# Optimization experiments

Hardware: AMD Instinct MI355X
Metric: run time of the kernel (lower is better)

The kernel has to match this reference:

```python
import jax, jax.numpy as jnp
import numpy as np

TAU = 2.0        # args.tau default (spikingjelly LIFNode)
V_TH = 1.0       # v_threshold
V_RESET = 0.0    # v_reset (hard reset)
ALPHA = 2.0      # ATan surrogate alpha

@jax.custom_vjp
def atan_spike(x):
    # Heaviside spike with ATan surrogate gradient (spikingjelly surrogate.ATan)
    return (x >= 0.0).astype(x.dtype)

def _atan_fwd(x):
    return atan_spike(x), x

def _atan_bwd(x, g):
    sg = (ALPHA / 2.0) / (1.0 + (jnp.pi / 2.0 * ALPHA * x) ** 2)
    return (g * sg,)

atan_spike.defvjp(_atan_fwd, _atan_bwd)

def setup_inputs() -> dict:
    key = jax.random.key(0)
    k1, k2, k3 = jax.random.split(key, 3)
    T, B, IN, OUT, NC = 16, 512, 3072, 2048, 10
    x_seq = jax.random.normal(k1, (T, B, IN), dtype=jnp.float32)
    # xavier-uniform-like scale: sqrt(2/(fan_in+fan_out))
    fc_w = jax.random.normal(k2, (OUT, IN), dtype=jnp.float32) * np.sqrt(2.0 / (IN + OUT)).astype(np.float32)
    fc_b = jnp.zeros((OUT,), jnp.float32)
    aux_w = jax.random.normal(k3, (NC, OUT), dtype=jnp.float32) * np.sqrt(2.0 / (OUT + NC)).astype(np.float32)
    aux_b = jnp.zeros((NC,), jnp.float32)
    return {"x_seq": x_seq, "fc_w": fc_w, "fc_b": fc_b, "aux_w": aux_w, "aux_b": aux_b}

def reference(x_seq, fc_w, fc_b, aux_w, aux_b):
    # fc over all timesteps: [T,B,in] @ [out,in]^T -> [T,B,out]
    cur_seq = jnp.einsum('tbi,oi->tbo', x_seq, fc_w) + fc_b

    def step(v, c):
        # LIF charge: v += (x - (v - v_reset)) / tau
        v = v + (c - (v - V_RESET)) / TAU
        s = atan_spike(v - V_TH)
        s_d = jax.lax.stop_gradient(s)  # detach_reset=True
        v = (1.0 - s_d) * v + s_d * V_RESET  # hard reset
        return v, s

    v0 = jnp.full(cur_seq.shape[1:], V_RESET, cur_seq.dtype)  # reset_net -> v = v_reset
    _, spk_seq = jax.lax.scan(step, v0, cur_seq)  # spk_seq: [T,B,out]
    count = spk_seq.sum(axis=0)                    # [B,out]
    logits = count @ aux_w.T + aux_b               # aux_head local logits [B,10]
    return spk_seq, count, logits
```

## Files before the change

### kernel.cpp

```cpp
#include <hip/hip_runtime.h>
#include <hip/hip_bf16.h>
#include <stdint.h>

#define T_   16
#define B_   512
#define IN_  3072
#define OUT_ 2048
#define NC_  10
#define M_   (T_ * B_)

#define BM 128
#define BN 128

#define SPK_SZ ((size_t)T_ * B_ * OUT_)
#define CNT_SZ ((size_t)B_ * OUT_)

#define TOL 1.2e-4
#define MAXFLAG (B_ * OUT_)

#define BK2   32
#define NCH2  (IN_ / BK2)
#define TILE_US 8192
#define APAN (M_ / BM)
#define BPAN (OUT_ / BN)

#define A_PREP_BLOCKS (APAN * NCH2 * 2)
#define B_PREP_BLOCKS (BPAN * NCH2 * 2)

typedef __attribute__((ext_vector_type(8))) short s16x8;
typedef __attribute__((ext_vector_type(4))) float f32x4;

__device__ unsigned int g_ctr;
__device__ unsigned int g_list[MAXFLAG];

__global__ void zero_ctr() { if (threadIdx.x == 0) g_ctr = 0; }

__device__ __forceinline__ unsigned short f2bf(float f) {
    __bf16 h = (__bf16)f;
    return *(unsigned short*)&h;
}
__device__ __forceinline__ float bf2f(unsigned short u) {
    union { unsigned int i; float f; } c; c.i = ((unsigned int)u) << 16; return c.f;
}
__device__ __forceinline__ int swz8(int r, int g) {
    return r * 64 + ((g ^ (r & 7)) << 3);
}

__device__ __forceinline__ void gload_lds16(const void* g, void* l) {
    __builtin_amdgcn_global_load_lds(
        (const __attribute__((address_space(1))) unsigned int*)g,
        (__attribute__((address_space(3))) unsigned int*)l, 16, 0, 0);
}

__global__ __launch_bounds__(256)
void prep2(const float* __restrict__ x, const float* __restrict__ w,
           unsigned short* __restrict__ Adig, unsigned short* __restrict__ Bdig)
{
    if (blockIdx.x == 0 && threadIdx.x == 0) g_ctr = 0;

    const float* src; unsigned short* dst; int id; bool isA;
    if (blockIdx.x < A_PREP_BLOCKS) {
        src = x; dst = Adig; id = blockIdx.x * 256 + threadIdx.x; isA = true;
    } else {
        src = w; dst = Bdig; id = (blockIdx.x - A_PREP_BLOCKS) * 256 + threadIdx.x; isA = false;
    }
    const int gk = id & 3;
    const int r  = (id >> 2) & 127;
    const int ch = (id >> 9) % NCH2;
    const int pa = id / (NCH2 * 512);
    const int m  = pa * 128 + r;
    const int k  = ch * BK2 + gk * 8;

    size_t srow;
    if (isA) srow = (size_t)(m & 15) * B_ + (m >> 4);
    else     srow = (size_t)m;

    float f[8];
    *(float4*)&f[0] = *(const float4*)(src + srow * IN_ + k);
    *(float4*)&f[4] = *(const float4*)(src + srow * IN_ + k + 4);
    s16x8 hi, lo;
#pragma unroll
    for (int j = 0; j < 8; ++j) {
        unsigned short hb = f2bf(f[j]);
        hi[j] = (short)hb;
        lo[j] = (short)f2bf(f[j] - bf2f(hb));
    }
    unsigned short* tb = dst + ((size_t)pa * NCH2 + ch) * TILE_US;
    *(s16x8*)&tb[swz8(r, gk)]     = hi;
    *(s16x8*)&tb[swz8(r, gk + 4)] = lo;
}

__global__ __launch_bounds__(256, 2)
void gemm_fused(const unsigned short* __restrict__ Adig,
                const unsigned short* __restrict__ Bdig,
                const float* __restrict__ fcb,
                float* __restrict__ out)
{
    __shared__ __align__(16) unsigned short SH[4 * TILE_US];
    unsigned short* Ash0 = SH;
    unsigned short* Bsh0 = SH + 2 * TILE_US;

    const int tid = threadIdx.x;
    const int l   = tid & 63;
    const int wv  = tid >> 6;
    const int wm  = (wv >> 1) * 64;
    const int wn  = (wv & 1) * 64;

    const int lin = blockIdx.x;
    const int xcd = lin & 7;
    const int jj  = lin >> 3;
    const int pm  = xcd * 8 + (jj & 7);
    const int pn  = jj >> 3;
    const int n0  = pn * BN;

    f32x4 acc[4][4];
#pragma unroll
    for (int i = 0; i < 4; ++i)
#pragma unroll
        for (int j = 0; j < 4; ++j) acc[i][j] = (f32x4)0.0f;

    const int lp = l & 15;
    const int lq = l >> 4;
    const int l8 = l * 8;

    const unsigned short* Abase = Adig + (size_t)pm * NCH2 * TILE_US;
    const unsigned short* Bbase = Bdig + (size_t)pn * NCH2 * TILE_US;

    auto stage = [&](int ch, int d) {
        if (wv < 2) {
            const unsigned short* sA = Abase + (size_t)ch * TILE_US + wv * 4096;
            unsigned short* dA = Ash0 + d * TILE_US + wv * 4096;
#pragma unroll
            for (int i = 0; i < 8; ++i)
                gload_lds16(sA + i * 512 + l8, dA + i * 512);
        } else {
            const unsigned short* sB = Bbase + (size_t)ch * TILE_US + (wv - 2) * 4096;
            unsigned short* dB = Bsh0 + d * TILE_US + (wv - 2) * 4096;
#pragma unroll
            for (int i = 0; i < 8; ++i)
                gload_lds16(sB + i * 512 + l8, dB + i * 512);
        }
    };

    stage(0, 0);

    for (int ch = 0; ch < NCH2; ++ch) {
        const int d = ch & 1;
        if (ch + 1 < NCH2) {
            stage(ch + 1, d ^ 1);
            asm volatile("s_waitcnt vmcnt(8)" ::: "memory");
        } else {
            asm volatile("s_waitcnt vmcnt(0)" ::: "memory");
        }
        __builtin_amdgcn_s_barrier();
        asm volatile("" ::: "memory");

        s16x8 a1f[4], a2f[4], b1f[4], b2f[4];
#pragma unroll
        for (int i = 0; i < 4; ++i) {
            const int ra = wm + i * 16 + lp;
            a1f[i] = *(const s16x8*)&Ash0[d * TILE_US + swz8(ra, lq)];
            a2f[i] = *(const s16x8*)&Ash0[d * TILE_US + swz8(ra, lq + 4)];
            const int rb = wn + i * 16 + lp;
            b1f[i] = *(const s16x8*)&Bsh0[d * TILE_US + swz8(rb, lq)];
            b2f[i] = *(const s16x8*)&Bsh0[d * TILE_US + swz8(rb, lq + 4)];
        }

        __builtin_amdgcn_s_setprio(1);
#pragma unroll
        for (int i = 0; i < 4; ++i)
#pragma unroll
            for (int j = 0; j < 4; ++j) {
                acc[i][j] = __builtin_amdgcn_mfma_f32_16x16x32_bf16(
                    a1f[i], b1f[j], acc[i][j], 0, 0, 0);
                acc[i][j] = __builtin_amdgcn_mfma_f32_16x16x32_bf16(
                    a2f[i], b1f[j], acc[i][j], 0, 0, 0);
                acc[i][j] = __builtin_amdgcn_mfma_f32_16x16x32_bf16(
                    a1f[i], b2f[j], acc[i][j], 0, 0, 0);
            }
        __builtin_amdgcn_s_setprio(0);

        asm volatile("s_waitcnt lgkmcnt(0)" ::: "memory");
        __builtin_amdgcn_s_barrier();
        asm volatile("" ::: "memory");
    }

    float* cf = (float*)SH;

    const int crow0 = lq * 4;
#pragma unroll
    for (int i = 0; i < 4; ++i)
#pragma unroll
        for (int j = 0; j < 4; ++j)
#pragma unroll
            for (int reg = 0; reg < 4; ++reg) {
                const int row = wm + i * 16 + crow0 + reg;
                const int col = wn + j * 16 + lp;
                cf[row * 128 + (col ^ ((row & 7) << 2))] = acc[i][j][reg];
            }
    __syncthreads();

    const int o_l = tid & 127;
    const int o   = n0 + o_l;
    const double bias = (double)fcb[o];
    const int bq0 = (tid >> 7) * 4;

#pragma unroll
    for (int q = 0; q < 4; ++q) {
        const int bl = bq0 + q;
        const int b  = pm * 8 + bl;
        double v = 0.0; int cnt = 0; bool fl = false;
#pragma unroll
        for (int t = 0; t < T_; ++t) {
            const int row = bl * 16 + t;
            const float c32 = cf[row * 128 + (o_l ^ ((row & 7) << 2))];
            const double c = (double)c32 + bias;
            v = v + (c - v) * 0.5;
            const double dlt = v - 1.0;
            const bool s = dlt >= 0.0;
            if (fabs(dlt) < TOL) fl = true;
            out[(size_t)t * CNT_SZ + (size_t)b * OUT_ + o] = s ? 1.0f : 0.0f;
            cnt += s ? 1 : 0;
            if (s) v = 0.0;
        }
        out[SPK_SZ + (size_t)b * OUT_ + o] = (float)cnt;
        if (fl) {
            unsigned int idx = atomicAdd(&g_ctr, 1u);
            if (idx < MAXFLAG) g_list[idx] = (unsigned int)(b * OUT_ + o);
        }
    }
}

__global__ __launch_bounds__(256, 2)
void gemm_split(const float* __restrict__ x, const float* __restrict__ w,
                float* __restrict__ cur)
{
    __shared__ __align__(16) unsigned short A1[BM * 64];
    __shared__ __align__(16) unsigned short A2[BM * 64];
    __shared__ __align__(16) unsigned short B1[BN * 64];
    __shared__ __align__(16) unsigned short B2[BN * 64];

    const int tid = threadIdx.x;
    const int l   = tid & 63;
    const int wv  = tid >> 6;
    const int wm  = (wv >> 1) * 64;
    const int wn  = (wv & 1) * 64;
    const int m0  = blockIdx.x * BM;
    const int n0  = blockIdx.y * BN;

    const int r = tid >> 1;
    const int h = tid & 1;
    const float* xa = x + (size_t)(m0 + r) * IN_ + h * 32;
    const float* wa = w + (size_t)(n0 + r) * IN_ + h * 32;

    f32x4 acc[4][4];
#pragma unroll
    for (int i = 0; i < 4; ++i)
#pragma unroll
        for (int j = 0; j < 4; ++j) acc[i][j] = (f32x4)0.0f;

    const int lp = l & 15;
    const int lq = l >> 4;

    for (int ch = 0; ch < 48; ++ch) {
        const int k0 = ch * 64;
        __syncthreads();
        float fx[32], fw[32];
#pragma unroll
        for (int i = 0; i < 8; ++i)
            *(float4*)&fx[4 * i] = *(const float4*)(xa + k0 + 4 * i);
#pragma unroll
        for (int i = 0; i < 8; ++i)
            *(float4*)&fw[4 * i] = *(const float4*)(wa + k0 + 4 * i);

#pragma unroll
        for (int q = 0; q < 4; ++q) {
            s16x8 vh, vl, uh, ul;
#pragma unroll
            for (int j = 0; j < 8; ++j) {
                float f = fx[8 * q + j];
                unsigned short hb = f2bf(f);
                vh[j] = (short)hb;
                vl[j] = (short)f2bf(f - bf2f(hb));
                float g = fw[8 * q + j];
                unsigned short gb = f2bf(g);
                uh[j] = (short)gb;
                ul[j] = (short)f2bf(g - bf2f(gb));
            }
            const int gg = h * 4 + q;
            *(s16x8*)&A1[swz8(r, gg)] = vh;
            *(s16x8*)&A2[swz8(r, gg)] = vl;
            *(s16x8*)&B1[swz8(r, gg)] = uh;
            *(s16x8*)&B2[swz8(r, gg)] = ul;
        }
        __syncthreads();

#pragma unroll
        for (int kk = 0; kk < 2; ++kk) {
            const int gb = kk * 4 + lq;
            s16x8 a1f[4], a2f[4], b1f[4], b2f[4];
#pragma unroll
            for (int i = 0; i < 4; ++i) {
                const int ra = wm + i * 16 + lp;
                a1f[i] = *(const s16x8*)&A1[swz8(ra, gb)];
                a2f[i] = *(const s16x8*)&A2[swz8(ra, gb)];
                const int rb = wn + i * 16 + lp;
                b1f[i] = *(const s16x8*)&B1[swz8(rb, gb)];
                b2f[i] = *(const s16x8*)&B2[swz8(rb, gb)];
            }
#pragma unroll
            for (int i = 0; i < 4; ++i)
#pragma unroll
                for (int j = 0; j < 4; ++j) {
                    acc[i][j] = __builtin_amdgcn_mfma_f32_16x16x32_bf16(
                        a1f[i], b1f[j], acc[i][j], 0, 0, 0);
                    acc[i][j] = __builtin_amdgcn_mfma_f32_16x16x32_bf16(
                        a2f[i], b1f[j], acc[i][j], 0, 0, 0);
                    acc[i][j] = __builtin_amdgcn_mfma_f32_16x16x32_bf16(
                        a1f[i], b2f[j], acc[i][j], 0, 0, 0);
                }
        }
    }

    const int crow = lq * 4, ccol = lp;
#pragma unroll
    for (int i = 0; i < 4; ++i)
#pragma unroll
        for (int j = 0; j < 4; ++j) {
            const size_t mbase = (size_t)(m0 + wm + i * 16 + crow);
            const int o = n0 + wn + j * 16 + ccol;
#pragma unroll
            for (int reg = 0; reg < 4; ++reg)
                cur[(mbase + reg) * OUT_ + o] = acc[i][j][reg];
        }
}

__global__ __launch_bounds__(256)
void lif_pass(const float* __restrict__ fcb, float* __restrict__ out)
{
    const int idx = blockIdx.x * 256 + threadIdx.x;
    const int o = idx & (OUT_ - 1);
    const double bias = (double)fcb[o];
    double v = 0.0; int cnt = 0; bool fl = false;
#pragma unroll
    for (int t = 0; t < T_; ++t) {
        const size_t p = (size_t)t * CNT_SZ + idx;
        double c = (double)out[p] + bias;
        v = v + (c - v) * 0.5;
        double d = v - 1.0;
        bool s = d >= 0.0;
        if (fabs(d) < TOL) fl = true;
        out[p] = s ? 1.0f : 0.0f;
        cnt += s ? 1 : 0;
        if (s) v = 0.0;
    }
    out[SPK_SZ + idx] = (float)cnt;
    if (fl) {
        unsigned int pI = atomicAdd(&g_ctr, 1u);
        if (pI < MAXFLAG) g_list[pI] = (unsigned int)idx;
    }
}

__global__ void fixup(const float* __restrict__ x, const float* __restrict__ w,
                      const float* __restrict__ fcb, float* __restrict__ out)
{
    int nf = (int)g_ctr; if (nf > MAXFLAG) nf = MAXFLAG;
    const int lane = threadIdx.x & 63;
    const int wid  = (blockIdx.x * blockDim.x + threadIdx.x) >> 6;
    const int nw   = (gridDim.x * blockDim.x) >> 6;

    for (int i = wid; i < nf; i += nw) {
        unsigned int e = g_list[i];
        int b = (int)(e >> 11), o = (int)(e & (OUT_ - 1));
        double part[T_];
#pragma unroll
        for (int t = 0; t < T_; ++t) part[t] = 0.0;
        const float* wrow = w + (size_t)o * IN_;
        for (int k = lane; k < IN_; k += 64) {
            double wvv = (double)wrow[k];
#pragma unroll
            for (int t = 0; t < T_; ++t)
                part[t] = fma((double)x[((size_t)t * B_ + b) * IN_ + k], wvv, part[t]);
        }
#pragma unroll
        for (int t = 0; t < T_; ++t)
#pragma unroll
            for (int off = 32; off > 0; off >>= 1)
                part[t] += __shfl_xor(part[t], off, 64);
        if (lane == 0) {
            double bias = (double)fcb[o];
            double v = 0.0; int cnt = 0;
#pragma unroll
            for (int t = 0; t < T_; ++t) {
                double c = part[t] + bias;
                v = v + (c - v) * 0.5;
                bool s = (v - 1.0) >= 0.0;
                out[(size_t)t * CNT_SZ + (size_t)b * OUT_ + o] = s ? 1.0f : 0.0f;
                cnt += s ? 1 : 0;
                if (s) v = 0.0;
            }
            out[SPK_SZ + (size_t)b * OUT_ + o] = (float)cnt;
        }
    }
}

__global__ void aux_logits(const float* __restrict__ cnt,
                           const float* __restrict__ aw,
                           const float* __restrict__ ab,
                           float* __restrict__ lg)
{
    const int b = blockIdx.x;
    const int lane = threadIdx.x;
    double p0=0,p1=0,p2=0,p3=0,p4=0,p5=0,p6=0,p7=0,p8=0,p9=0;
    for (int o = lane; o < OUT_; o += 64) {
        double c = (double)cnt[(size_t)b * OUT_ + o];
        p0 = fma(c, (double)aw[0 * OUT_ + o], p0);
        p1 = fma(c, (double)aw[1 * OUT_ + o], p1);
        p2 = fma(c, (double)aw[2 * OUT_ + o], p2);
        p3 = fma(c, (double)aw[3 * OUT_ + o], p3);
        p4 = fma(c, (double)aw[4 * OUT_ + o], p4);
        p5 = fma(c, (double)aw[5 * OUT_ + o], p5);
        p6 = fma(c, (double)aw[6 * OUT_ + o], p6);
        p7 = fma(c, (double)aw[7 * OUT_ + o], p7);
        p8 = fma(c, (double)aw[8 * OUT_ + o], p8);
        p9 = fma(c, (double)aw[9 * OUT_ + o], p9);
    }
#pragma unroll
    for (int off = 32; off > 0; off >>= 1) {
        p0 += __shfl_xor(p0, off, 64); p1 += __shfl_xor(p1, off, 64);
        p2 += __shfl_xor(p2, off, 64); p3 += __shfl_xor(p3, off, 64);
        p4 += __shfl_xor(p4, off, 64); p5 += __shfl_xor(p5, off, 64);
        p6 += __shfl_xor(p6, off, 64); p7 += __shfl_xor(p7, off, 64);
        p8 += __shfl_xor(p8, off, 64); p9 += __shfl_xor(p9, off, 64);
    }
    if (lane == 0) {
        double pv[NC_] = {p0,p1,p2,p3,p4,p5,p6,p7,p8,p9};
#pragma unroll
        for (int c = 0; c < NC_; ++c)
            lg[(size_t)b * NC_ + c] = (float)(pv[c] + (double)ab[c]);
    }
}

extern "C" void kernel_launch(void* const* d_in, const int* in_sizes, int n_in,
                              void* d_out, int out_size, void* d_ws, size_t ws_size,
                              hipStream_t stream)
{
    (void)in_sizes; (void)n_in; (void)out_size;
    const float* x   = (const float*)d_in[0];
    const float* w   = (const float*)d_in[1];
    const float* fcb = (const float*)d_in[2];
    const float* aw  = (const float*)d_in[3];
    const float* ab  = (const float*)d_in[4];
    float* out = (float*)d_out;

    const size_t needA = (size_t)APAN * NCH2 * TILE_US * 2;
    const size_t needB = (size_t)BPAN * NCH2 * TILE_US * 2;

    if (ws_size >= needA + needB) {
        unsigned short* Adig = (unsigned short*)d_ws;
        unsigned short* Bdig = Adig + (size_t)APAN * NCH2 * TILE_US;
        prep2<<<dim3(A_PREP_BLOCKS + B_PREP_BLOCKS), dim3(256), 0, stream>>>(
            x, w, Adig, Bdig);
        gemm_fused<<<dim3(APAN * BPAN), dim3(256), 0, stream>>>(Adig, Bdig, fcb, out);
    } else {
        zero_ctr<<<dim3(1), dim3(64), 0, stream>>>();
        gemm_split<<<dim3(M_ / BM, OUT_ / BN), dim3(256), 0, stream>>>(x, w, out);
        lif_pass<<<dim3(CNT_SZ / 256), dim3(256), 0, stream>>>(fcb, out);
    }

    fixup<<<dim3(512), dim3(256), 0, stream>>>(x, w, fcb, out);

    aux_logits<<<dim3(B_), dim3(64), 0, stream>>>(
        out + SPK_SZ, aw, ab, out + SPK_SZ + CNT_SZ);
}
```

Before: 358.7 us.

## Enlarge fused GEMM tile to 256x256 with 512-thread blocks

Each block of the fused split-bf16 GEMM now computes a 256x256 output tile with 8 waves instead of 128x128 with 4. Each wave covers 128 rows by 64 columns, loads B fragments one column block at a time, and staging is spread evenly over all waves. The intent is to halve global/L2 traffic per FLOP and raise MFMA work per LDS load. The LIF epilogue runs in two halves through the shared scratch buffer. The cost is a larger accumulator register footprint, 1 block per CU, and only 256 blocks, which hurts occupancy and load balance across 256 CUs.

```diff
diff --git a/kernel.cpp b/kernel.cpp
--- a/kernel.cpp
+++ b/kernel.cpp
@@ -90,32 +90,32 @@
     *(s16x8*)&tb[swz8(r, gk + 4)] = lo;
 }
 
-__global__ __launch_bounds__(256, 2)
+__global__ __launch_bounds__(512, 1)
 void gemm_fused(const unsigned short* __restrict__ Adig,
                 const unsigned short* __restrict__ Bdig,
                 const float* __restrict__ fcb,
                 float* __restrict__ out)
 {
-    __shared__ __align__(16) unsigned short SH[4 * TILE_US];
-    unsigned short* Ash0 = SH;
-    unsigned short* Bsh0 = SH + 2 * TILE_US;
+    __shared__ __align__(16) unsigned short SH[2 * 4 * TILE_US];
 
     const int tid = threadIdx.x;
     const int l   = tid & 63;
     const int wv  = tid >> 6;
-    const int wm  = (wv >> 1) * 64;
-    const int wn  = (wv & 1) * 64;
+    const int wh  = wv >> 2;
+    const int wn  = (wv & 3) * 64;
+    const int pB  = (wv >> 1) & 1;
+    const int rb0 = (wv & 1) * 64;
 
     const int lin = blockIdx.x;
     const int xcd = lin & 7;
     const int jj  = lin >> 3;
-    const int pm  = xcd * 8 + (jj & 7);
-    const int pn  = jj >> 3;
-    const int n0  = pn * BN;
-
-    f32x4 acc[4][4];
-#pragma unroll
-    for (int i = 0; i < 4; ++i)
+    const int pm2 = xcd * 4 + (jj & 3);
+    const int pn2 = jj >> 2;
+    const int n0  = pn2 * 256;
+
+    f32x4 acc[8][4];
+#pragma unroll
+    for (int i = 0; i < 8; ++i)
 #pragma unroll
         for (int j = 0; j < 4; ++j) acc[i][j] = (f32x4)0.0f;
 
@@ -123,23 +123,18 @@
     const int lq = l >> 4;
     const int l8 = l * 8;
 
-    const unsigned short* Abase = Adig + (size_t)pm * NCH2 * TILE_US;
-    const unsigned short* Bbase = Bdig + (size_t)pn * NCH2 * TILE_US;
+    const int rg  = wv >> 1;
+    const int sub = (wv & 1) * 4096;
+    const unsigned short* gsrc0;
+    if (rg < 2) gsrc0 = Adig + ((size_t)(2 * pm2 + rg) * NCH2) * TILE_US;
+    else        gsrc0 = Bdig + ((size_t)(2 * pn2 + rg - 2) * NCH2) * TILE_US;
 
     auto stage = [&](int ch, int d) {
-        if (wv < 2) {
-            const unsigned short* sA = Abase + (size_t)ch * TILE_US + wv * 4096;
-            unsigned short* dA = Ash0 + d * TILE_US + wv * 4096;
-#pragma unroll
-            for (int i = 0; i < 8; ++i)
-                gload_lds16(sA + i * 512 + l8, dA + i * 512);
-        } else {
-            const unsigned short* sB = Bbase + (size_t)ch * TILE_US + (wv - 2) * 4096;
-            unsigned short* dB = Bsh0 + d * TILE_US + (wv - 2) * 4096;
-#pragma unroll
-            for (int i = 0; i < 8; ++i)
-                gload_lds16(sB + i * 512 + l8, dB + i * 512);
-        }
+        const unsigned short* s = gsrc0 + (size_t)ch * TILE_US + sub;
+        unsigned short* dp = SH + (d * 4 + rg) * TILE_US + sub;
+#pragma unroll
+        for (int i = 0; i < 8; ++i)
+            gload_lds16(s + i * 512 + l8, dp + i * 512);
     };
 
     stage(0, 0);
@@ -155,29 +150,32 @@
         __builtin_amdgcn_s_barrier();
         asm volatile("" ::: "memory");
 
-        s16x8 a1f[4], a2f[4], b1f[4], b2f[4];
-#pragma unroll
-        for (int i = 0; i < 4; ++i) {
-            const int ra = wm + i * 16 + lp;
-            a1f[i] = *(const s16x8*)&Ash0[d * TILE_US + swz8(ra, lq)];
-            a2f[i] = *(const s16x8*)&Ash0[d * TILE_US + swz8(ra, lq + 4)];
-            const int rb = wn + i * 16 + lp;
-            b1f[i] = *(const s16x8*)&Bsh0[d * TILE_US + swz8(rb, lq)];
-            b2f[i] = *(const s16x8*)&Bsh0[d * TILE_US + swz8(rb, lq + 4)];
-        }
-
+        const unsigned short* Ap = SH + (d * 4 + wh) * TILE_US;
+        const unsigned short* Bp = SH + (d * 4 + 2 + pB) * TILE_US;
+
+        s16x8 a1f[8], a2f[8];
+#pragma unroll
+        for (int i = 0; i < 8; ++i) {
+            const int ra = i * 16 + lp;
+            a1f[i] = *(const s16x8*)&Ap[swz8(ra, lq)];
+            a2f[i] = *(const s16x8*)&Ap[swz8(ra, lq + 4)];
+        }
         __builtin_amdgcn_s_setprio(1);
 #pragma unroll
-        for (int i = 0; i < 4; ++i)
-#pragma unroll
-            for (int j = 0; j < 4; ++j) {
+        for (int j = 0; j < 4; ++j) {
+            const int rb = rb0 + j * 16 + lp;
+            const s16x8 b1f = *(const s16x8*)&Bp[swz8(rb, lq)];
+            const s16x8 b2f = *(const s16x8*)&Bp[swz8(rb, lq + 4)];
+#pragma unroll
+            for (int i = 0; i < 8; ++i) {
                 acc[i][j] = __builtin_amdgcn_mfma_f32_16x16x32_bf16(
-                    a1f[i], b1f[j], acc[i][j], 0, 0, 0);
+                    a1f[i], b1f, acc[i][j], 0, 0, 0);
                 acc[i][j] = __builtin_amdgcn_mfma_f32_16x16x32_bf16(
-                    a2f[i], b1f[j], acc[i][j], 0, 0, 0);
+                    a2f[i], b1f, acc[i][j], 0, 0, 0);
                 acc[i][j] = __builtin_amdgcn_mfma_f32_16x16x32_bf16(
-                    a1f[i], b2f[j], acc[i][j], 0, 0, 0);
-            }
+                    a1f[i], b2f, acc[i][j], 0, 0, 0);
+            }
+        }
         __builtin_amdgcn_s_setprio(0);
 
         asm volatile("s_waitcnt lgkmcnt(0)" ::: "memory");
@@ -187,46 +185,50 @@
 
     float* cf = (float*)SH;
 
-    const int crow0 = lq * 4;
-#pragma unroll
-    for (int i = 0; i < 4; ++i)
-#pragma unroll
-        for (int j = 0; j < 4; ++j)
-#pragma unroll
-            for (int reg = 0; reg < 4; ++reg) {
-                const int row = wm + i * 16 + crow0 + reg;
-                const int col = wn + j * 16 + lp;
-                cf[row * 128 + (col ^ ((row & 7) << 2))] = acc[i][j][reg];
-            }
-    __syncthreads();
-
-    const int o_l = tid & 127;
+    const int o_l = tid & 255;
     const int o   = n0 + o_l;
     const double bias = (double)fcb[o];
-    const int bq0 = (tid >> 7) * 4;
-
-#pragma unroll
-    for (int q = 0; q < 4; ++q) {
-        const int bl = bq0 + q;
-        const int b  = pm * 8 + bl;
-        double v = 0.0; int cnt = 0; bool fl = false;
-#pragma unroll
-        for (int t = 0; t < T_; ++t) {
-            const int row = bl * 16 + t;
-            const float c32 = cf[row * 128 + (o_l ^ ((row & 7) << 2))];
-            const double c = (double)c32 + bias;
-            v = v + (c - v) * 0.5;
-            const double dlt = v - 1.0;
-            const bool s = dlt >= 0.0;
-            if (fabs(dlt) < TOL) fl = true;
-            out[(size_t)t * CNT_SZ + (size_t)b * OUT_ + o] = s ? 1.0f : 0.0f;
-            cnt += s ? 1 : 0;
-            if (s) v = 0.0;
-        }
-        out[SPK_SZ + (size_t)b * OUT_ + o] = (float)cnt;
-        if (fl) {
-            unsigned int idx = atomicAdd(&g_ctr, 1u);
-            if (idx < MAXFLAG) g_list[idx] = (unsigned int)(b * OUT_ + o);
+    const int bq0 = (tid >> 8) * 4;
+
+    for (int p = 0; p < 2; ++p) {
+        if (p) __syncthreads();
+        if (wh == p) {
+#pragma unroll
+            for (int i = 0; i < 8; ++i)
+#pragma unroll
+                for (int j = 0; j < 4; ++j)
+#pragma unroll
+                    for (int reg = 0; reg < 4; ++reg) {
+                        const int row = i * 16 + lq * 4 + reg;
+                        const int col = wn + j * 16 + lp;
+                        cf[row * 256 + (col ^ ((row & 12) << 1))] = acc[i][j][reg];
+                    }
+        }
+        __syncthreads();
+
+#pragma unroll
+        for (int q = 0; q < 4; ++q) {
+            const int rl = bq0 + q;
+            const int b  = pm2 * 16 + p * 8 + rl;
+            double v = 0.0; int cnt = 0; bool fl = false;
+#pragma unroll
+            for (int t = 0; t < T_; ++t) {
+                const int row = rl * 16 + t;
+                const float c32 = cf[row * 256 + (o_l ^ ((row & 12) << 1))];
+                const double c = (double)c32 + bias;
+                v = v + (c - v) * 0.5;
+                const double dlt = v - 1.0;
+                const bool s = dlt >= 0.0;
+                if (fabs(dlt) < TOL) fl = true;
+                out[(size_t)t * CNT_SZ + (size_t)b * OUT_ + o] = s ? 1.0f : 0.0f;
+                cnt += s ? 1 : 0;
+                if (s) v = 0.0;
+            }
+            out[SPK_SZ + (size_t)b * OUT_ + o] = (float)cnt;
+            if (fl) {
+                unsigned int idx = atomicAdd(&g_ctr, 1u);
+                if (idx < MAXFLAG) g_list[idx] = (unsigned int)(b * OUT_ + o);
+            }
         }
     }
 }
@@ -461,7 +463,7 @@
         unsigned short* Bdig = Adig + (size_t)APAN * NCH2 * TILE_US;
         prep2<<<dim3(A_PREP_BLOCKS + B_PREP_BLOCKS), dim3(256), 0, stream>>>(
             x, w, Adig, Bdig);
-        gemm_fused<<<dim3(APAN * BPAN), dim3(256), 0, stream>>>(Adig, Bdig, fcb, out);
+        gemm_fused<<<dim3(256), dim3(512), 0, stream>>>(Adig, Bdig, fcb, out);
     } else {
         zero_ctr<<<dim3(1), dim3(64), 0, stream>>>();
         gemm_split<<<dim3(M_ / BM, OUT_ / BN), dim3(256), 0, stream>>>(x, w, out);
```

After: 354.5 us. About the same (-1.2%).
